# Performance work log

Hardware: AMD Instinct MI355X
Metric: run time of the kernel (lower is better)

Reference implementation:

```python
import jax, jax.numpy as jnp
import numpy as np
from math import sqrt


def setup_inputs() -> dict:
    key0 = jax.random.key(0)
    ks = jax.random.split(key0, 7)
    N, H, E, D, S = 32, 16, 128, 128, 2047
    return {
        "query": jax.random.normal(ks[0], (N, H, E), dtype=jnp.float32),
        "key": jax.random.normal(ks[1], (N, H, E), dtype=jnp.float32),
        "value": jax.random.normal(ks[2], (N, H, D), dtype=jnp.float32),
        "keys_cache": jax.random.normal(ks[3], (N, H, S, E), dtype=jnp.float32),
        "values_cache": jax.random.normal(ks[4], (N, H, S, D), dtype=jnp.float32),
        "w_pre": jax.random.normal(ks[5], (H, H), dtype=jnp.float32) * (1.0 / sqrt(H)),
        "w_post": jax.random.normal(ks[6], (H, H), dtype=jnp.float32) * (1.0 / sqrt(H)),
    }


def reference(query, key, value, keys_cache, values_cache, w_pre, w_post):
    # Single recurrent decode step with talking-heads mixing (dropout in eval mode).
    N, H, E = query.shape
    softmax_temp = 1.0 / sqrt(E)
    # Append current key/value to the cache: [N,H,S+1,E] / [N,H,S+1,D]
    keys = jnp.concatenate([keys_cache, key[:, :, None, :]], axis=2)
    values = jnp.concatenate([values_cache, value[:, :, None, :]], axis=2)
    # Scores: [N,H,S]
    QK = jnp.einsum('nhe,nhse->nhs', query, keys)
    # Pre-softmax talking heads (1x1 conv over head axis): out_g = sum_h w[g,h] * in_h
    QK = jnp.einsum('gh,nhs->ngs', w_pre, QK)
    A = jax.nn.softmax(softmax_temp * QK, axis=-1)
    # Post-softmax talking heads
    A = jnp.einsum('gh,nhs->ngs', w_post, A)
    # Weighted value readout: [N,H,D]
    V = jnp.einsum('nhs,nhsd->nhd', A, values)
    return V, keys, values
```

## Files before the change

kernel.cpp:

```cpp
#include <hip/hip_runtime.h>
#include <cstddef>

constexpr int N_  = 32;
constexpr int H_  = 16;
constexpr int E_  = 128;
constexpr int D_  = 128;
constexpr int S_  = 2047;
constexpr int SP1 = 2048;
constexpr int NH  = N_ * H_;

constexpr int ROWS_PER_BLOCK = 256;
constexpr int CHUNKS = SP1 / ROWS_PER_BLOCK;
constexpr int COLCH  = SP1 / 256;

typedef float vfloat4 __attribute__((ext_vector_type(4)));

__global__ __launch_bounds__(256) void k1_keys_scores(
    const float* __restrict__ query, const float* __restrict__ key,
    const float* __restrict__ keys_cache,
    float* __restrict__ keys_out, float* __restrict__ scores)
{
  __shared__ float sc[ROWS_PER_BLOCK];
  const int bid   = blockIdx.x;
  const int nh    = bid / CHUNKS;
  const int chunk = bid % CHUNKS;
  const int tid   = threadIdx.x;
  const int wave  = tid >> 6;
  const int lane  = tid & 63;
  const int half  = lane >> 5;
  const int lcol  = lane & 31;
  const int rbase = wave * 64 + half;

  const vfloat4 q4 = *reinterpret_cast<const vfloat4*>(query + (size_t)nh * E_ + lcol * 4);

  #pragma unroll 8
  for (int it = 0; it < 32; ++it) {
    const int r = rbase + it * 2;
    const int s = chunk * ROWS_PER_BLOCK + r;
    const float* src = (s < S_) ? (keys_cache + ((size_t)nh * S_ + s) * E_)
                                : (key + (size_t)nh * E_);
    vfloat4 k4 = *reinterpret_cast<const vfloat4*>(src + lcol * 4);
    __builtin_nontemporal_store(k4,
        reinterpret_cast<vfloat4*>(keys_out + ((size_t)nh * SP1 + s) * E_ + lcol * 4));

    float p = q4.x * k4.x + q4.y * k4.y + q4.z * k4.z + q4.w * k4.w;
    p += __shfl_xor(p, 1);
    p += __shfl_xor(p, 2);
    p += __shfl_xor(p, 4);
    p += __shfl_xor(p, 8);
    p += __shfl_xor(p, 16);
    if (lcol == 0) sc[r] = p;
  }
  __syncthreads();
  scores[(size_t)nh * SP1 + chunk * ROWS_PER_BLOCK + tid] = sc[tid];
}

__global__ __launch_bounds__(256) void k2a_stats(
    const float* __restrict__ scores, const float* __restrict__ w_pre,
    float* __restrict__ blkstats)
{
  __shared__ float wp[H_ * H_];
  __shared__ float red[4][H_];
  __shared__ float bmax[H_];
  const int n   = blockIdx.x >> 3;
  const int cc  = blockIdx.x & 7;
  const int tid = threadIdx.x;
  const int wave = tid >> 6;
  const int lane = tid & 63;
  const float temp = 0.08838834764831845f;

  wp[tid] = w_pre[tid];
  __syncthreads();

  const float* base = scores + (size_t)n * H_ * SP1 + cc * 256 + tid;
  float sc[H_];
  #pragma unroll
  for (int h = 0; h < H_; ++h) sc[h] = base[(size_t)h * SP1];

  float mx[H_];
  #pragma unroll
  for (int g = 0; g < H_; ++g) {
    float acc = 0.0f;
    #pragma unroll
    for (int h = 0; h < H_; ++h) acc += wp[g * H_ + h] * sc[h];
    mx[g] = acc * temp;
  }

  #pragma unroll
  for (int g = 0; g < H_; ++g) {
    float v = mx[g];
    #pragma unroll
    for (int m = 1; m <= 32; m <<= 1) v = fmaxf(v, __shfl_xor(v, m));
    if (lane == 0) red[wave][g] = v;
  }
  __syncthreads();
  if (tid < H_) {
    float v = fmaxf(fmaxf(red[0][tid], red[1][tid]), fmaxf(red[2][tid], red[3][tid]));
    bmax[tid] = v;
    blkstats[((size_t)(n * COLCH + cc) * 2 + 0) * H_ + tid] = v;
  }
  __syncthreads();

  #pragma unroll
  for (int g = 0; g < H_; ++g) {
    float e = __expf(mx[g] - bmax[g]);
    #pragma unroll
    for (int m = 1; m <= 32; m <<= 1) e += __shfl_xor(e, m);
    if (lane == 0) red[wave][g] = e;
  }
  __syncthreads();
  if (tid < H_) {
    blkstats[((size_t)(n * COLCH + cc) * 2 + 1) * H_ + tid] =
        red[0][tid] + red[1][tid] + red[2][tid] + red[3][tid];
  }
}

__global__ __launch_bounds__(256) void k2c_a2(
    const float* __restrict__ scores, const float* __restrict__ blkstats,
    const float* __restrict__ w_pre, const float* __restrict__ w_post,
    float* __restrict__ a2out)
{
  __shared__ float wp[H_ * H_];
  __shared__ float wq[H_ * H_];
  __shared__ float mg[H_];
  __shared__ float ig[H_];
  const int n   = blockIdx.x >> 3;
  const int cc  = blockIdx.x & 7;
  const int tid = threadIdx.x;
  const float temp = 0.08838834764831845f;

  wp[tid] = w_pre[tid];
  wq[tid] = w_post[tid];
  if (tid < H_) {
    float bm[COLCH], bs[COLCH];
    #pragma unroll
    for (int c = 0; c < COLCH; ++c) {
      bm[c] = blkstats[((size_t)(n * COLCH + c) * 2 + 0) * H_ + tid];
      bs[c] = blkstats[((size_t)(n * COLCH + c) * 2 + 1) * H_ + tid];
    }
    float m = bm[0];
    #pragma unroll
    for (int c = 1; c < COLCH; ++c) m = fmaxf(m, bm[c]);
    float den = 0.0f;
    #pragma unroll
    for (int c = 0; c < COLCH; ++c) den += bs[c] * __expf(bm[c] - m);
    mg[tid] = m;
    ig[tid] = 1.0f / den;
  }
  __syncthreads();

  const float* base = scores + (size_t)n * H_ * SP1 + cc * 256 + tid;
  float sc[H_];
  #pragma unroll
  for (int h = 0; h < H_; ++h) sc[h] = base[(size_t)h * SP1];

  float P[H_];
  #pragma unroll
  for (int h = 0; h < H_; ++h) {
    float acc = 0.0f;
    #pragma unroll
    for (int h2 = 0; h2 < H_; ++h2) acc += wp[h * H_ + h2] * sc[h2];
    P[h] = __expf(acc * temp - mg[h]) * ig[h];
  }

  #pragma unroll
  for (int g = 0; g < H_; ++g) {
    float a = 0.0f;
    #pragma unroll
    for (int h = 0; h < H_; ++h) a += wq[g * H_ + h] * P[h];
    a2out[((size_t)(n * H_ + g)) * SP1 + cc * 256 + tid] = a;
  }
}

__global__ __launch_bounds__(256) void k3_values(
    const float* __restrict__ value, const float* __restrict__ values_cache,
    const float* __restrict__ a2buf, float* __restrict__ values_out,
    float* __restrict__ partials)
{
  __shared__ float lds[8][128];
  __shared__ float a2[ROWS_PER_BLOCK];
  const int bid   = blockIdx.x;
  const int nh    = bid / CHUNKS;
  const int chunk = bid % CHUNKS;
  const int tid   = threadIdx.x;
  const int wave  = tid >> 6;
  const int lane  = tid & 63;
  const int half  = lane >> 5;
  const int lcol  = lane & 31;
  const int group = wave * 2 + half;
  const int rbase = wave * 64 + half;

  a2[tid] = a2buf[(size_t)nh * SP1 + chunk * ROWS_PER_BLOCK + tid];
  __syncthreads();

  float accx = 0.0f, accy = 0.0f, accz = 0.0f, accw = 0.0f;

  #pragma unroll 8
  for (int it = 0; it < 32; ++it) {
    const int r = rbase + it * 2;
    const int s = chunk * ROWS_PER_BLOCK + r;
    const float* src = (s < S_) ? (values_cache + ((size_t)nh * S_ + s) * D_)
                                : (value + (size_t)nh * D_);
    vfloat4 v4 = *reinterpret_cast<const vfloat4*>(src + lcol * 4);
    __builtin_nontemporal_store(v4,
        reinterpret_cast<vfloat4*>(values_out + ((size_t)nh * SP1 + s) * D_ + lcol * 4));

    const float w = a2[r];
    accx += w * v4.x;
    accy += w * v4.y;
    accz += w * v4.z;
    accw += w * v4.w;
  }

  lds[group][lcol * 4 + 0] = accx;
  lds[group][lcol * 4 + 1] = accy;
  lds[group][lcol * 4 + 2] = accz;
  lds[group][lcol * 4 + 3] = accw;
  __syncthreads();
  if (tid < 128) {
    float sum = 0.0f;
    #pragma unroll
    for (int gq = 0; gq < 8; ++gq) sum += lds[gq][tid];
    partials[(size_t)bid * 128 + tid] = sum;
  }
}

__global__ __launch_bounds__(256) void k4_reduce(
    const float* __restrict__ partials, float* __restrict__ v_out)
{
  const int g = blockIdx.x * 256 + threadIdx.x;
  const int nh = g >> 7;
  const int d = g & 127;
  float s = 0.0f;
  #pragma unroll
  for (int c = 0; c < CHUNKS; ++c)
    s += partials[((size_t)(nh * CHUNKS + c)) * 128 + d];
  v_out[g] = s;
}

extern "C" void kernel_launch(void* const* d_in, const int* in_sizes, int n_in,
                              void* d_out, int out_size, void* d_ws, size_t ws_size,
                              hipStream_t stream) {
  const float* query        = (const float*)d_in[0];
  const float* key          = (const float*)d_in[1];
  const float* value        = (const float*)d_in[2];
  const float* keys_cache   = (const float*)d_in[3];
  const float* values_cache = (const float*)d_in[4];
  const float* w_pre        = (const float*)d_in[5];
  const float* w_post       = (const float*)d_in[6];

  float* out = (float*)d_out;
  float* v_out      = out;
  float* keys_out   = out + (size_t)NH * D_;
  float* values_out = keys_out + (size_t)NH * SP1 * E_;

  float* buf0     = (float*)d_ws;
  float* a2buf    = buf0 + (size_t)NH * SP1;
  float* blkstats = a2buf + (size_t)NH * SP1;
  float* partials = blkstats + (size_t)N_ * COLCH * 2 * H_;

  k1_keys_scores<<<NH * CHUNKS, 256, 0, stream>>>(query, key, keys_cache,
                                                  keys_out, buf0);
  k2a_stats<<<N_ * COLCH, 256, 0, stream>>>(buf0, w_pre, blkstats);
  k2c_a2<<<N_ * COLCH, 256, 0, stream>>>(buf0, blkstats, w_pre, w_post, a2buf);
  k3_values<<<NH * CHUNKS, 256, 0, stream>>>(value, values_cache, a2buf,
                                             values_out, partials);
  k4_reduce<<<(NH * 128) / 256, 256, 0, stream>>>(partials, v_out);
}
```

Before: 433.4 us.

## Fuse final reduction into values kernel via last-block atomic counter

Removes the separate k4_reduce launch: each k3 block writes its partial sums, bumps a per-(n,h) atomic counter, and the last block to arrive sums the partials and writes the output. The counters are cleared with a memset on the stream, which adds one operation in place of the removed kernel launch. The key and value cache copies also switch from nontemporal stores to plain vector stores, which changes how the large output writes interact with the caches.

```diff
diff --git a/kernel.cpp b/kernel.cpp
--- a/kernel.cpp
+++ b/kernel.cpp
@@ -40,8 +40,7 @@
     const float* src = (s < S_) ? (keys_cache + ((size_t)nh * S_ + s) * E_)
                                 : (key + (size_t)nh * E_);
     vfloat4 k4 = *reinterpret_cast<const vfloat4*>(src + lcol * 4);
-    __builtin_nontemporal_store(k4,
-        reinterpret_cast<vfloat4*>(keys_out + ((size_t)nh * SP1 + s) * E_ + lcol * 4));
+    *reinterpret_cast<vfloat4*>(keys_out + ((size_t)nh * SP1 + s) * E_ + lcol * 4) = k4;
 
     float p = q4.x * k4.x + q4.y * k4.y + q4.z * k4.z + q4.w * k4.w;
     p += __shfl_xor(p, 1);
@@ -175,10 +174,12 @@
 __global__ __launch_bounds__(256) void k3_values(
     const float* __restrict__ value, const float* __restrict__ values_cache,
     const float* __restrict__ a2buf, float* __restrict__ values_out,
-    float* __restrict__ partials)
+    float* __restrict__ partials, int* __restrict__ ctr,
+    float* __restrict__ v_out)
 {
   __shared__ float lds[8][128];
   __shared__ float a2[ROWS_PER_BLOCK];
+  __shared__ int lastflag;
   const int bid   = blockIdx.x;
   const int nh    = bid / CHUNKS;
   const int chunk = bid % CHUNKS;
@@ -202,8 +203,7 @@
     const float* src = (s < S_) ? (values_cache + ((size_t)nh * S_ + s) * D_)
                                 : (value + (size_t)nh * D_);
     vfloat4 v4 = *reinterpret_cast<const vfloat4*>(src + lcol * 4);
-    __builtin_nontemporal_store(v4,
-        reinterpret_cast<vfloat4*>(values_out + ((size_t)nh * SP1 + s) * D_ + lcol * 4));
+    *reinterpret_cast<vfloat4*>(values_out + ((size_t)nh * SP1 + s) * D_ + lcol * 4) = v4;
 
     const float w = a2[r];
     accx += w * v4.x;
@@ -221,21 +221,26 @@
     float sum = 0.0f;
     #pragma unroll
     for (int gq = 0; gq < 8; ++gq) sum += lds[gq][tid];
-    partials[(size_t)bid * 128 + tid] = sum;
-  }
-}
-
-__global__ __launch_bounds__(256) void k4_reduce(
-    const float* __restrict__ partials, float* __restrict__ v_out)
-{
-  const int g = blockIdx.x * 256 + threadIdx.x;
-  const int nh = g >> 7;
-  const int d = g & 127;
-  float s = 0.0f;
-  #pragma unroll
-  for (int c = 0; c < CHUNKS; ++c)
-    s += partials[((size_t)(nh * CHUNKS + c)) * 128 + d];
-  v_out[g] = s;
+    __hip_atomic_store(&partials[(size_t)bid * 128 + tid], sum,
+                       __ATOMIC_RELAXED, __HIP_MEMORY_SCOPE_AGENT);
+  }
+  __syncthreads();
+
+  if (tid == 0) {
+    const int old = __hip_atomic_fetch_add(&ctr[nh], 1, __ATOMIC_ACQ_REL,
+                                           __HIP_MEMORY_SCOPE_AGENT);
+    lastflag = (old == CHUNKS - 1);
+  }
+  __syncthreads();
+
+  if (lastflag && tid < 128) {
+    float s = 0.0f;
+    #pragma unroll
+    for (int c = 0; c < CHUNKS; ++c)
+      s += __hip_atomic_load(&partials[((size_t)(nh * CHUNKS + c)) * 128 + tid],
+                             __ATOMIC_RELAXED, __HIP_MEMORY_SCOPE_AGENT);
+    v_out[(size_t)nh * 128 + tid] = s;
+  }
 }
 
 extern "C" void kernel_launch(void* const* d_in, const int* in_sizes, int n_in,
@@ -258,12 +263,14 @@
   float* a2buf    = buf0 + (size_t)NH * SP1;
   float* blkstats = a2buf + (size_t)NH * SP1;
   float* partials = blkstats + (size_t)N_ * COLCH * 2 * H_;
+  int*   ctrs     = (int*)(partials + (size_t)NH * CHUNKS * 128);
+
+  hipMemsetAsync(ctrs, 0, NH * sizeof(int), stream);
 
   k1_keys_scores<<<NH * CHUNKS, 256, 0, stream>>>(query, key, keys_cache,
                                                   keys_out, buf0);
   k2a_stats<<<N_ * COLCH, 256, 0, stream>>>(buf0, w_pre, blkstats);
   k2c_a2<<<N_ * COLCH, 256, 0, stream>>>(buf0, blkstats, w_pre, w_post, a2buf);
   k3_values<<<NH * CHUNKS, 256, 0, stream>>>(value, values_cache, a2buf,
-                                             values_out, partials);
-  k4_reduce<<<(NH * 128) / 256, 256, 0, stream>>>(partials, v_out);
-}
+                                             values_out, partials, ctrs, v_out);
+}
```

Measured after the change: 689.9 us. 59.2% more time.
